# Kernel tuning notes

Measured on AMD Instinct MI355X. Metric: run time of the kernel, lower is better.

## Reference

```python
import jax, jax.numpy as jnp
import numpy as np

N_NODES = 50000
N_EDGES = 800000
IN_CH, HID_CH, OUT_CH = 128, 256, 128


def _linear_init(key, fan_in, fan_out):
    # torch nn.Linear default: U(-1/sqrt(fan_in), 1/sqrt(fan_in)) for W and b
    kw, kb = jax.random.split(key)
    bound = 1.0 / np.sqrt(fan_in)
    W = jax.random.uniform(kw, (fan_in, fan_out), jnp.float32, -bound, bound)
    b = jax.random.uniform(kb, (fan_out,), jnp.float32, -bound, bound)
    return W, b


def setup_inputs() -> dict:
    key = jax.random.key(0)
    ks = jax.random.split(key, 8)
    x = jax.random.normal(ks[0], (N_NODES, IN_CH), jnp.float32)
    edge_index = jax.random.randint(ks[1], (2, N_EDGES), 0, N_NODES, jnp.int64)
    W1a, b1a = _linear_init(ks[2], IN_CH, HID_CH)
    W1b, b1b = _linear_init(ks[3], HID_CH, HID_CH)
    W2, b2 = _linear_init(ks[4], HID_CH, HID_CH)
    W3, b3 = _linear_init(ks[5], HID_CH, OUT_CH)
    eps1 = jnp.zeros((), jnp.float32)  # train_eps=True, init 0
    return {
        "x": x, "edge_index": edge_index,
        "W1a": W1a, "b1a": b1a, "W1b": W1b, "b1b": b1b, "eps1": eps1,
        "W2": W2, "b2": b2, "W3": W3, "b3": b3,
    }


def _gin_aggregate(h, edge_index):
    # PyG: messages flow source (row 0) -> target (row 1); sum aggregation
    src, dst = edge_index[0], edge_index[1]
    return jax.ops.segment_sum(h[src], dst, num_segments=N_NODES)


def reference(x, edge_index, W1a, b1a, W1b, b1b, eps1, W2, b2, W3, b3):
    # conv1: mlp1((1+eps1)*x + sum_neighbors(x)), mlp1 = Lin-ReLU-Lin-ReLU
    z = (1.0 + eps1) * x + _gin_aggregate(x, edge_index)
    h = jax.nn.relu(z @ W1a + b1a)
    h = jax.nn.relu(h @ W1b + b1b)
    h = jax.nn.relu(h)  # outer .relu() (no-op after ReLU, kept for fidelity)
    # conv2: eps fixed at 0 -> (1+0)*h + agg; mlp2 = Lin-ReLU
    z2 = h + _gin_aggregate(h, edge_index)
    h2 = jax.nn.relu(z2 @ W2 + b2)
    h2 = jax.nn.relu(h2)
    return h2 @ W3 + b3
```

## Files before the change

### kernel.cpp

```cpp
#include <hip/hip_runtime.h>


typedef __attribute__((ext_vector_type(8))) short bf16x8;
typedef __attribute__((ext_vector_type(4))) float f32x4;

__device__ __forceinline__ float bf2f(unsigned short u) {
  unsigned v = ((unsigned)u) << 16;
  return __builtin_bit_cast(float, v);
}
__device__ __forceinline__ unsigned short f2bf(float f) {
  unsigned u = __builtin_bit_cast(unsigned, f);
  u += 0x7fffu + ((u >> 16) & 1u);
  return (unsigned short)(u >> 16);
}

__device__ __forceinline__ void async16(const void* g, void* l) {
  __builtin_amdgcn_global_load_lds(
      (const __attribute__((address_space(1))) void*)g,
      (__attribute__((address_space(3))) void*)l, 16, 0, 0);
}

static const int NN     = 50000;
static const int NE     = 800000;
static const int NB_E   = 196;
static const int SCAN_N = 256 * NB_E;
static const int SCAN_NB = 49;
static const int CSR_CAP = 6144;

__global__ __launch_bounds__(256) void k_prep(
    const float* __restrict__ W1a, const float* __restrict__ W1b,
    const float* __restrict__ W2,  const float* __restrict__ W3,
    unsigned short* __restrict__ WT,
    const float* __restrict__ x, unsigned short* __restrict__ xb)
{
  int idx = blockIdx.x * 256 + threadIdx.x;
  if (idx < 196608) {
    const float* W; unsigned short* out; int K, N, li = idx;
    if (li < 32768)        { W = W1a; out = WT;          K = 128; N = 256; }
    else if (li < 98304)   { W = W1b; out = WT + 32768;  K = 256; N = 256; li -= 32768; }
    else if (li < 163840)  { W = W2;  out = WT + 98304;  K = 256; N = 256; li -= 98304; }
    else                   { W = W3;  out = WT + 163840; K = 256; N = 128; li -= 163840; }
    int n = li / K, k = li - n * K;
    out[li] = f2bf(W[k * N + n]);
  } else if (idx < 196608 + NN * 32) {
    int i = idx - 196608;
    float4 v = reinterpret_cast<const float4*>(x)[i];
    ushort4 b; b.x = f2bf(v.x); b.y = f2bf(v.y); b.z = f2bf(v.z); b.w = f2bf(v.w);
    reinterpret_cast<ushort4*>(xb)[i] = b;
  }
}

__global__ __launch_bounds__(256) void k_hist1(const int* __restrict__ ei,
    int* __restrict__ sc)
{
  __shared__ int h[256];
  const int t = threadIdx.x, k = blockIdx.x;
  h[t] = 0;
  __syncthreads();
  const int4* dv4 = reinterpret_cast<const int4*>(ei + NE);
#pragma unroll
  for (int j = 0; j < 4; j++) {
    int e4 = k * 1024 + j * 256 + t;
    if (e4 < NE / 4) {
      int4 d = dv4[e4];
      atomicAdd(&h[d.x >> 8], 1);
      atomicAdd(&h[d.y >> 8], 1);
      atomicAdd(&h[d.z >> 8], 1);
      atomicAdd(&h[d.w >> 8], 1);
    }
  }
  __syncthreads();
  sc[t * NB_E + k] = h[t];
}

__global__ __launch_bounds__(1024) void k_scan_a(int* __restrict__ sc,
    int* __restrict__ bsum)
{
  __shared__ int sh[1024];
  const int t = threadIdx.x;
  int idx = blockIdx.x * 1024 + t;
  int c = (idx < SCAN_N) ? sc[idx] : 0;
  sh[t] = c;
  __syncthreads();
  int v = c;
  for (int off = 1; off < 1024; off <<= 1) {
    int tmp = (t >= off) ? sh[t - off] : 0;
    __syncthreads();
    v += tmp; sh[t] = v;
    __syncthreads();
  }
  if (idx < SCAN_N) sc[idx] = v - c;
  if (t == 1023) bsum[blockIdx.x] = v;
}

__global__ __launch_bounds__(1024) void k_scan_b(const int* __restrict__ bsum,
    int* __restrict__ sc)
{
  __shared__ int sb[64];
  const int t = threadIdx.x;
  if (t < SCAN_NB) sb[t] = bsum[t];
  __syncthreads();
  int base = 0;
  for (int j = 0; j < SCAN_NB; j++) base += (j < (int)blockIdx.x) ? sb[j] : 0;
  int idx = blockIdx.x * 1024 + t;
  if (idx < SCAN_N) sc[idx] += base;
}

__global__ __launch_bounds__(256) void k_binscat(const int* __restrict__ ei,
    const int* __restrict__ sc, int* __restrict__ tmp)
{
  __shared__ int base[256];
  __shared__ int cur[256];
  const int t = threadIdx.x, k = blockIdx.x;
  base[t] = sc[t * NB_E + k];
  cur[t] = 0;
  __syncthreads();
  const int4* sv4 = reinterpret_cast<const int4*>(ei);
  const int4* dv4 = reinterpret_cast<const int4*>(ei + NE);
#pragma unroll
  for (int j = 0; j < 4; j++) {
    int e4 = k * 1024 + j * 256 + t;
    if (e4 < NE / 4) {
      int4 s = sv4[e4];
      int4 d = dv4[e4];
      int b0 = d.x >> 8, p0 = atomicAdd(&cur[b0], 1);
      tmp[base[b0] + p0] = ((d.x & 255) << 16) | s.x;
      int b1 = d.y >> 8, p1 = atomicAdd(&cur[b1], 1);
      tmp[base[b1] + p1] = ((d.y & 255) << 16) | s.y;
      int b2 = d.z >> 8, p2 = atomicAdd(&cur[b2], 1);
      tmp[base[b2] + p2] = ((d.z & 255) << 16) | s.z;
      int b3 = d.w >> 8, p3 = atomicAdd(&cur[b3], 1);
      tmp[base[b3] + p3] = ((d.w & 255) << 16) | s.w;
    }
  }
}

__global__ __launch_bounds__(256) void k_csr(const int* __restrict__ sc,
    const int* __restrict__ tmp, int* __restrict__ offs, int* __restrict__ srcs)
{
  __shared__ int pk[CSR_CAP];
  __shared__ int lh[256];
  __shared__ int lo[256];
  __shared__ int cur[256];
  const int t = threadIdx.x, b = blockIdx.x;
  int ebeg = sc[b * NB_E];
  int eend = sc[(b + 1) * NB_E];
  int cnt = eend - ebeg;
  if (cnt > CSR_CAP) cnt = CSR_CAP;
  lh[t] = 0;
  __syncthreads();
  for (int i = t; i < cnt; i += 256) {
    int v = tmp[ebeg + i];
    pk[i] = v;
    atomicAdd(&lh[(v >> 16) & 255], 1);
  }
  __syncthreads();
  int x = lh[t];
  lo[t] = x;
  __syncthreads();
  for (int off = 1; off < 256; off <<= 1) {
    int y = (t >= off) ? lo[t - off] : 0;
    __syncthreads();
    lo[t] += y;
    __syncthreads();
  }
  int excl = lo[t] - x;
  int g = b * 256 + t;
  if (g <= NN) offs[g] = ebeg + excl;
  cur[t] = excl;
  __syncthreads();
  for (int i = t; i < cnt; i += 256) {
    int v = pk[i];
    int local = (v >> 16) & 255;
    int p = atomicAdd(&cur[local], 1);
    srcs[ebeg + p] = v & 0xFFFF;
  }
}

template<int C, bool L1>
__global__ __launch_bounds__(256) void k_gather(const int* __restrict__ offs,
    const int* __restrict__ srcs, const unsigned short* __restrict__ feat,
    const float* __restrict__ selfx, const float* __restrict__ eps,
    unsigned short* __restrict__ out)
{
  constexpr int TPN = C / 8;
  int tid = blockIdx.x * 256 + threadIdx.x;
  int node = tid / TPN;
  if (node >= NN) return;
  int c0 = (tid % TPN) * 8;

  float a[8];
  if (L1) {
    float sc_ = 1.0f + eps[0];
    const float* sp = selfx + (size_t)node * C + c0;
    f32x4 v0 = __builtin_nontemporal_load(reinterpret_cast<const f32x4*>(sp));
    f32x4 v1 = __builtin_nontemporal_load(reinterpret_cast<const f32x4*>(sp + 4));
    a[0] = v0.x * sc_; a[1] = v0.y * sc_; a[2] = v0.z * sc_; a[3] = v0.w * sc_;
    a[4] = v1.x * sc_; a[5] = v1.y * sc_; a[6] = v1.z * sc_; a[7] = v1.w * sc_;
  } else {
    bf16x8 v = *reinterpret_cast<const bf16x8*>(feat + (size_t)node * C + c0);
#pragma unroll
    for (int j = 0; j < 8; j++) a[j] = bf2f((unsigned short)v[j]);
  }

  int beg = __builtin_nontemporal_load(offs + node);
  int end = __builtin_nontemporal_load(offs + node + 1);
  int i = beg;
  for (; i + 4 <= end; i += 4) {
    int s0 = __builtin_nontemporal_load(srcs + i);
    int s1 = __builtin_nontemporal_load(srcs + i + 1);
    int s2 = __builtin_nontemporal_load(srcs + i + 2);
    int s3 = __builtin_nontemporal_load(srcs + i + 3);
    bf16x8 v0 = *reinterpret_cast<const bf16x8*>(feat + (size_t)s0 * C + c0);
    bf16x8 v1 = *reinterpret_cast<const bf16x8*>(feat + (size_t)s1 * C + c0);
    bf16x8 v2 = *reinterpret_cast<const bf16x8*>(feat + (size_t)s2 * C + c0);
    bf16x8 v3 = *reinterpret_cast<const bf16x8*>(feat + (size_t)s3 * C + c0);
#pragma unroll
    for (int j = 0; j < 8; j++) a[j] += bf2f((unsigned short)v0[j]);
#pragma unroll
    for (int j = 0; j < 8; j++) a[j] += bf2f((unsigned short)v1[j]);
#pragma unroll
    for (int j = 0; j < 8; j++) a[j] += bf2f((unsigned short)v2[j]);
#pragma unroll
    for (int j = 0; j < 8; j++) a[j] += bf2f((unsigned short)v3[j]);
  }
  for (; i < end; ++i) {
    int s0 = __builtin_nontemporal_load(srcs + i);
    bf16x8 v0 = *reinterpret_cast<const bf16x8*>(feat + (size_t)s0 * C + c0);
#pragma unroll
    for (int j = 0; j < 8; j++) a[j] += bf2f((unsigned short)v0[j]);
  }

  bf16x8 o;
#pragma unroll
  for (int j = 0; j < 8; j++) o[j] = (short)f2bf(a[j]);
  __builtin_nontemporal_store(o,
      reinterpret_cast<bf16x8*>(out + (size_t)node * C + c0));
}

template<int CIN, int COUT, bool RELU_OUT, bool OUT_F32>
__global__ __launch_bounds__(1024) void k_mlp(
    const unsigned short* __restrict__ A,
    const unsigned short* __restrict__ B1T,
    const float* __restrict__ bias1,
    const unsigned short* __restrict__ B2T,
    const float* __restrict__ bias2,
    unsigned short* __restrict__ outB, float* __restrict__ outF, int M)
{
  constexpr int LDH = 264;
  __shared__ unsigned short Asb[2][128 * 32];
  __shared__ unsigned short Bsb[2][256 * 32];
  __shared__ unsigned short Hs[128 * LDH];

  const int tid = threadIdx.x;
  const int w = tid >> 6, l = tid & 63;
  const int bm = blockIdx.x * 128;
  const int lr = l >> 2;
  const int lc = (l & 3) * 8;

  auto stageA = [&](int buf, int kt) {
    if (w < 8) {
      int tr = w * 16;
      int ar = bm + tr + lr; if (ar >= M) ar = M - 1;
      async16(A + (size_t)ar * CIN + kt + lc, &Asb[buf][tr * 32]);
    }
    {
      int tr = w * 16;
      async16(B1T + (size_t)(tr + lr) * CIN + kt + lc, &Bsb[buf][tr * 32]);
    }
  };
  auto stageB = [&](int buf, int kt) {
    if (w < COUT / 16) {
      int tr = w * 16;
      async16(B2T + (size_t)(tr + lr) * 256 + kt + lc, &Bsb[buf][tr * 32]);
    }
  };

  const int wrA = w >> 3, wcA = w & 7;
  f32x4 accA[4][2];
#pragma unroll
  for (int m = 0; m < 4; m++)
#pragma unroll
    for (int n = 0; n < 2; n++) accA[m][n] = (f32x4)(0.0f);

  stageA(0, 0);
  __syncthreads();
  int cur = 0;
  for (int kt = 0; kt < CIN; kt += 32) {
    if (kt + 32 < CIN) stageA(cur ^ 1, kt + 32);
    bf16x8 af[4], bfr[2];
#pragma unroll
    for (int m = 0; m < 4; m++)
      af[m] = *reinterpret_cast<const bf16x8*>(
          &Asb[cur][(wrA * 64 + m * 16 + (l & 15)) * 32 + (l >> 4) * 8]);
#pragma unroll
    for (int n = 0; n < 2; n++)
      bfr[n] = *reinterpret_cast<const bf16x8*>(
          &Bsb[cur][(wcA * 32 + n * 16 + (l & 15)) * 32 + (l >> 4) * 8]);
#pragma unroll
    for (int m = 0; m < 4; m++)
#pragma unroll
      for (int n = 0; n < 2; n++)
        accA[m][n] = __builtin_amdgcn_mfma_f32_16x16x32_bf16(
            af[m], bfr[n], accA[m][n], 0, 0, 0);
    __syncthreads();
    cur ^= 1;
  }

  stageB(0, 0);
#pragma unroll
  for (int m = 0; m < 4; m++) {
    int row0 = wrA * 64 + m * 16 + ((l >> 4) << 2);
#pragma unroll
    for (int n = 0; n < 2; n++) {
      int col = wcA * 32 + n * 16 + (l & 15);
      float bv = bias1[col];
#pragma unroll
      for (int r = 0; r < 4; r++) {
        float v = fmaxf(accA[m][n][r] + bv, 0.0f);
        Hs[(row0 + r) * LDH + col] = f2bf(v);
      }
    }
  }
  __syncthreads();

  constexpr int NWC = COUT / 32;
  constexpr int NWR = 16 / NWC;
  constexpr int RPW = 128 / NWR;
  constexpr int MF  = RPW / 16;
  const int wrB = w / NWC, wcB = w % NWC;

  f32x4 accB[MF][2];
#pragma unroll
  for (int m = 0; m < MF; m++)
#pragma unroll
    for (int n = 0; n < 2; n++) accB[m][n] = (f32x4)(0.0f);

  cur = 0;
  for (int kt = 0; kt < 256; kt += 32) {
    if (kt + 32 < 256) stageB(cur ^ 1, kt + 32);
    bf16x8 af[MF], bfr[2];
#pragma unroll
    for (int m = 0; m < MF; m++)
      af[m] = *reinterpret_cast<const bf16x8*>(
          &Hs[(wrB * RPW + m * 16 + (l & 15)) * LDH + kt + (l >> 4) * 8]);
#pragma unroll
    for (int n = 0; n < 2; n++)
      bfr[n] = *reinterpret_cast<const bf16x8*>(
          &Bsb[cur][(wcB * 32 + n * 16 + (l & 15)) * 32 + (l >> 4) * 8]);
#pragma unroll
    for (int m = 0; m < MF; m++)
#pragma unroll
      for (int n = 0; n < 2; n++)
        accB[m][n] = __builtin_amdgcn_mfma_f32_16x16x32_bf16(
            af[m], bfr[n], accB[m][n], 0, 0, 0);
    __syncthreads();
    cur ^= 1;
  }

#pragma unroll
  for (int m = 0; m < MF; m++) {
    int row0 = bm + wrB * RPW + m * 16 + ((l >> 4) << 2);
#pragma unroll
    for (int n = 0; n < 2; n++) {
      int col = wcB * 32 + n * 16 + (l & 15);
      float bv = bias2[col];
#pragma unroll
      for (int r = 0; r < 4; r++) {
        int row = row0 + r;
        if (row < M) {
          float v = accB[m][n][r] + bv;
          if (RELU_OUT) v = fmaxf(v, 0.0f);
          if (OUT_F32) outF[(size_t)row * COUT + col] = v;
          else         outB[(size_t)row * COUT + col] = f2bf(v);
        }
      }
    }
  }
}

static const size_t OFF_XB   = 0;
static const size_t OFF_Z1B  = 12800000;
static const size_t OFF_HB   = 25600000;
static const size_t OFF_Z2B  = 51200000;
static const size_t OFF_SC   = 76800000;
static const size_t OFF_BSUM = 77000704;
static const size_t OFF_TMP  = 77000960;
static const size_t OFF_SRC  = 80200960;
static const size_t OFF_OFFS = 83400960;
static const size_t OFF_WT   = 83601024;

extern "C" void kernel_launch(void* const* d_in, const int* in_sizes, int n_in,
                              void* d_out, int out_size, void* d_ws, size_t ws_size,
                              hipStream_t stream)
{
  const float* x    = (const float*)d_in[0];
  const int*   ei   = (const int*)d_in[1];
  const float* W1a  = (const float*)d_in[2];
  const float* b1a  = (const float*)d_in[3];
  const float* W1b  = (const float*)d_in[4];
  const float* b1b  = (const float*)d_in[5];
  const float* eps1 = (const float*)d_in[6];
  const float* W2   = (const float*)d_in[7];
  const float* b2   = (const float*)d_in[8];
  const float* W3   = (const float*)d_in[9];
  const float* b3   = (const float*)d_in[10];

  char* ws = (char*)d_ws;
  unsigned short* xb   = (unsigned short*)(ws + OFF_XB);
  unsigned short* z1b  = (unsigned short*)(ws + OFF_Z1B);
  unsigned short* hb   = (unsigned short*)(ws + OFF_HB);
  unsigned short* z2b  = (unsigned short*)(ws + OFF_Z2B);
  int*            sc   = (int*)(ws + OFF_SC);
  int*            bsum = (int*)(ws + OFF_BSUM);
  int*            tmp  = (int*)(ws + OFF_TMP);
  int*            srcs = (int*)(ws + OFF_SRC);
  int*            offs = (int*)(ws + OFF_OFFS);
  unsigned short* wt   = (unsigned short*)(ws + OFF_WT);
  unsigned short* w1at = wt;
  unsigned short* w1bt = wt + 32768;
  unsigned short* w2t  = wt + 98304;
  unsigned short* w3t  = wt + 163840;

  k_prep<<<(196608 + NN * 32 + 255) / 256, 256, 0, stream>>>(
      W1a, W1b, W2, W3, wt, x, xb);
  k_hist1<<<NB_E, 256, 0, stream>>>(ei, sc);
  k_scan_a<<<SCAN_NB, 1024, 0, stream>>>(sc, bsum);
  k_scan_b<<<SCAN_NB, 1024, 0, stream>>>(bsum, sc);
  k_binscat<<<NB_E, 256, 0, stream>>>(ei, sc, tmp);
  k_csr<<<NB_E, 256, 0, stream>>>(sc, tmp, offs, srcs);

  k_gather<128, true><<<NN * 16 / 256, 256, 0, stream>>>(
      offs, srcs, xb, x, eps1, z1b);
  k_mlp<128, 256, true, false><<<391, 1024, 0, stream>>>(
      z1b, w1at, b1a, w1bt, b1b, hb, nullptr, NN);

  k_gather<256, false><<<NN * 32 / 256, 256, 0, stream>>>(
      offs, srcs, hb, nullptr, nullptr, z2b);
  k_mlp<256, 128, false, true><<<391, 1024, 0, stream>>>(
      z2b, w2t, b2, w3t, b3, nullptr, (float*)d_out, NN);
}
```

Measured before the change: 193.1 us.

## Fuse histogram into prep, fold scan fixup into consumers, halve MLP tile

Merges the edge-histogram kernel into the weight/feature conversion kernel and removes the separate scan-fixup kernel. Consumers now add the block prefix sums from bsum on the fly, which cuts two launches from the CSR build. The MLP kernels drop to 64-row tiles with 512 threads and twice as many blocks, which lowers shared memory per block and may raise occupancy. In exchange, each block re-reads the B weights for half as many rows, so weight traffic per output row doubles.

```diff
diff --git a/kernel.cpp b/kernel.cpp
--- a/kernel.cpp
+++ b/kernel.cpp
@@ -20,10 +20,10 @@
       (__attribute__((address_space(3))) void*)l, 16, 0, 0);
 }
 
-static const int NN     = 50000;
-static const int NE     = 800000;
-static const int NB_E   = 196;
-static const int SCAN_N = 256 * NB_E;
+static const int NN      = 50000;
+static const int NE      = 800000;
+static const int NB_E    = 196;
+static const int SCAN_N  = 256 * NB_E;
 static const int SCAN_NB = 49;
 static const int CSR_CAP = 6144;
 
@@ -31,9 +31,32 @@
     const float* __restrict__ W1a, const float* __restrict__ W1b,
     const float* __restrict__ W2,  const float* __restrict__ W3,
     unsigned short* __restrict__ WT,
-    const float* __restrict__ x, unsigned short* __restrict__ xb)
-{
-  int idx = blockIdx.x * 256 + threadIdx.x;
+    const float* __restrict__ x, unsigned short* __restrict__ xb,
+    const int* __restrict__ ei, int* __restrict__ sc)
+{
+  __shared__ int h[256];
+  const int t = threadIdx.x;
+  if (blockIdx.x < NB_E) {
+    const int k = blockIdx.x;
+    h[t] = 0;
+    __syncthreads();
+    const int4* dv4 = reinterpret_cast<const int4*>(ei + NE);
+#pragma unroll
+    for (int j = 0; j < 4; j++) {
+      int e4 = k * 1024 + j * 256 + t;
+      if (e4 < NE / 4) {
+        int4 d = dv4[e4];
+        atomicAdd(&h[d.x >> 8], 1);
+        atomicAdd(&h[d.y >> 8], 1);
+        atomicAdd(&h[d.z >> 8], 1);
+        atomicAdd(&h[d.w >> 8], 1);
+      }
+    }
+    __syncthreads();
+    sc[t * NB_E + k] = h[t];
+    return;
+  }
+  int idx = (blockIdx.x - NB_E) * 256 + t;
   if (idx < 196608) {
     const float* W; unsigned short* out; int K, N, li = idx;
     if (li < 32768)        { W = W1a; out = WT;          K = 128; N = 256; }
@@ -50,29 +73,6 @@
   }
 }
 
-__global__ __launch_bounds__(256) void k_hist1(const int* __restrict__ ei,
-    int* __restrict__ sc)
-{
-  __shared__ int h[256];
-  const int t = threadIdx.x, k = blockIdx.x;
-  h[t] = 0;
-  __syncthreads();
-  const int4* dv4 = reinterpret_cast<const int4*>(ei + NE);
-#pragma unroll
-  for (int j = 0; j < 4; j++) {
-    int e4 = k * 1024 + j * 256 + t;
-    if (e4 < NE / 4) {
-      int4 d = dv4[e4];
-      atomicAdd(&h[d.x >> 8], 1);
-      atomicAdd(&h[d.y >> 8], 1);
-      atomicAdd(&h[d.z >> 8], 1);
-      atomicAdd(&h[d.w >> 8], 1);
-    }
-  }
-  __syncthreads();
-  sc[t * NB_E + k] = h[t];
-}
-
 __global__ __launch_bounds__(1024) void k_scan_a(int* __restrict__ sc,
     int* __restrict__ bsum)
 {
@@ -93,27 +93,24 @@
   if (t == 1023) bsum[blockIdx.x] = v;
 }
 
-__global__ __launch_bounds__(1024) void k_scan_b(const int* __restrict__ bsum,
-    int* __restrict__ sc)
-{
-  __shared__ int sb[64];
-  const int t = threadIdx.x;
-  if (t < SCAN_NB) sb[t] = bsum[t];
-  __syncthreads();
-  int base = 0;
-  for (int j = 0; j < SCAN_NB; j++) base += (j < (int)blockIdx.x) ? sb[j] : 0;
-  int idx = blockIdx.x * 1024 + t;
-  if (idx < SCAN_N) sc[idx] += base;
-}
-
 __global__ __launch_bounds__(256) void k_binscat(const int* __restrict__ ei,
-    const int* __restrict__ sc, int* __restrict__ tmp)
+    const int* __restrict__ sc, const int* __restrict__ bsum,
+    int* __restrict__ tmp)
 {
   __shared__ int base[256];
   __shared__ int cur[256];
+  __shared__ int sb[SCAN_NB];
   const int t = threadIdx.x, k = blockIdx.x;
-  base[t] = sc[t * NB_E + k];
+  if (t < SCAN_NB) sb[t] = bsum[t];
   cur[t] = 0;
+  __syncthreads();
+  {
+    int idx = t * NB_E + k;
+    int nb = idx >> 10;
+    int pre = 0;
+    for (int j = 0; j < nb; j++) pre += sb[j];
+    base[t] = sc[idx] + pre;
+  }
   __syncthreads();
   const int4* sv4 = reinterpret_cast<const int4*>(ei);
   const int4* dv4 = reinterpret_cast<const int4*>(ei + NE);
@@ -136,18 +133,28 @@
 }
 
 __global__ __launch_bounds__(256) void k_csr(const int* __restrict__ sc,
-    const int* __restrict__ tmp, int* __restrict__ offs, int* __restrict__ srcs)
+    const int* __restrict__ bsum, const int* __restrict__ tmp,
+    int* __restrict__ offs, int* __restrict__ srcs)
 {
   __shared__ int pk[CSR_CAP];
   __shared__ int lh[256];
   __shared__ int lo[256];
   __shared__ int cur[256];
+  __shared__ int sb[SCAN_NB];
   const int t = threadIdx.x, b = blockIdx.x;
-  int ebeg = sc[b * NB_E];
-  int eend = sc[(b + 1) * NB_E];
+  if (t < SCAN_NB) sb[t] = bsum[t];
+  lh[t] = 0;
+  __syncthreads();
+  int i0 = b * NB_E, i1 = (b + 1) * NB_E;
+  int p0 = 0, p1 = 0;
+  for (int j = 0; j < SCAN_NB; j++) {
+    p0 += (j < (i0 >> 10)) ? sb[j] : 0;
+    p1 += (j < (i1 >> 10)) ? sb[j] : 0;
+  }
+  int ebeg = sc[i0] + p0;
+  int eend = sc[i1] + p1;
   int cnt = eend - ebeg;
   if (cnt > CSR_CAP) cnt = CSR_CAP;
-  lh[t] = 0;
   __syncthreads();
   for (int i = t; i < cnt; i += 256) {
     int v = tmp[ebeg + i];
@@ -171,8 +178,7 @@
   __syncthreads();
   for (int i = t; i < cnt; i += 256) {
     int v = pk[i];
-    int local = (v >> 16) & 255;
-    int p = atomicAdd(&cur[local], 1);
+    int p = atomicAdd(&cur[(v >> 16) & 255], 1);
     srcs[ebeg + p] = v & 0xFFFF;
   }
 }
@@ -239,7 +245,7 @@
 }
 
 template<int CIN, int COUT, bool RELU_OUT, bool OUT_F32>
-__global__ __launch_bounds__(1024) void k_mlp(
+__global__ __launch_bounds__(512) void k_mlp(
     const unsigned short* __restrict__ A,
     const unsigned short* __restrict__ B1T,
     const float* __restrict__ bias1,
@@ -248,35 +254,36 @@
     unsigned short* __restrict__ outB, float* __restrict__ outF, int M)
 {
   constexpr int LDH = 264;
-  __shared__ unsigned short Asb[2][128 * 32];
+  __shared__ unsigned short Asb[2][64 * 32];
   __shared__ unsigned short Bsb[2][256 * 32];
-  __shared__ unsigned short Hs[128 * LDH];
+  __shared__ unsigned short Hs[64 * LDH];
 
   const int tid = threadIdx.x;
   const int w = tid >> 6, l = tid & 63;
-  const int bm = blockIdx.x * 128;
+  const int bm = blockIdx.x * 64;
   const int lr = l >> 2;
   const int lc = (l & 3) * 8;
 
   auto stageA = [&](int buf, int kt) {
-    if (w < 8) {
+    if (w < 4) {
       int tr = w * 16;
       int ar = bm + tr + lr; if (ar >= M) ar = M - 1;
       async16(A + (size_t)ar * CIN + kt + lc, &Asb[buf][tr * 32]);
     }
-    {
-      int tr = w * 16;
+#pragma unroll
+    for (int ch = w; ch < 16; ch += 8) {
+      int tr = ch * 16;
       async16(B1T + (size_t)(tr + lr) * CIN + kt + lc, &Bsb[buf][tr * 32]);
     }
   };
   auto stageB = [&](int buf, int kt) {
-    if (w < COUT / 16) {
-      int tr = w * 16;
+#pragma unroll
+    for (int ch = w; ch < COUT / 16; ch += 8) {
+      int tr = ch * 16;
       async16(B2T + (size_t)(tr + lr) * 256 + kt + lc, &Bsb[buf][tr * 32]);
     }
   };
 
-  const int wrA = w >> 3, wcA = w & 7;
   f32x4 accA[4][2];
 #pragma unroll
   for (int m = 0; m < 4; m++)
@@ -292,11 +299,11 @@
 #pragma unroll
     for (int m = 0; m < 4; m++)
       af[m] = *reinterpret_cast<const bf16x8*>(
-          &Asb[cur][(wrA * 64 + m * 16 + (l & 15)) * 32 + (l >> 4) * 8]);
+          &Asb[cur][(m * 16 + (l & 15)) * 32 + (l >> 4) * 8]);
 #pragma unroll
     for (int n = 0; n < 2; n++)
       bfr[n] = *reinterpret_cast<const bf16x8*>(
-          &Bsb[cur][(wcA * 32 + n * 16 + (l & 15)) * 32 + (l >> 4) * 8]);
+          &Bsb[cur][(w * 32 + n * 16 + (l & 15)) * 32 + (l >> 4) * 8]);
 #pragma unroll
     for (int m = 0; m < 4; m++)
 #pragma unroll
@@ -310,10 +317,10 @@
   stageB(0, 0);
 #pragma unroll
   for (int m = 0; m < 4; m++) {
-    int row0 = wrA * 64 + m * 16 + ((l >> 4) << 2);
+    int row0 = m * 16 + ((l >> 4) << 2);
 #pragma unroll
     for (int n = 0; n < 2; n++) {
-      int col = wcA * 32 + n * 16 + (l & 15);
+      int col = w * 32 + n * 16 + (l & 15);
       float bv = bias1[col];
 #pragma unroll
       for (int r = 0; r < 4; r++) {
@@ -325,8 +332,8 @@
   __syncthreads();
 
   constexpr int NWC = COUT / 32;
-  constexpr int NWR = 16 / NWC;
-  constexpr int RPW = 128 / NWR;
+  constexpr int NWR = 8 / NWC;
+  constexpr int RPW = 64 / NWR;
   constexpr int MF  = RPW / 16;
   const int wrB = w / NWC, wcB = w % NWC;
 
@@ -422,21 +429,19 @@
   unsigned short* w2t  = wt + 98304;
   unsigned short* w3t  = wt + 163840;
 
-  k_prep<<<(196608 + NN * 32 + 255) / 256, 256, 0, stream>>>(
-      W1a, W1b, W2, W3, wt, x, xb);
-  k_hist1<<<NB_E, 256, 0, stream>>>(ei, sc);
+  k_prep<<<NB_E + (196608 + NN * 32 + 255) / 256, 256, 0, stream>>>(
+      W1a, W1b, W2, W3, wt, x, xb, ei, sc);
   k_scan_a<<<SCAN_NB, 1024, 0, stream>>>(sc, bsum);
-  k_scan_b<<<SCAN_NB, 1024, 0, stream>>>(bsum, sc);
-  k_binscat<<<NB_E, 256, 0, stream>>>(ei, sc, tmp);
-  k_csr<<<NB_E, 256, 0, stream>>>(sc, tmp, offs, srcs);
+  k_binscat<<<NB_E, 256, 0, stream>>>(ei, sc, bsum, tmp);
+  k_csr<<<NB_E, 256, 0, stream>>>(sc, bsum, tmp, offs, srcs);
 
   k_gather<128, true><<<NN * 16 / 256, 256, 0, stream>>>(
       offs, srcs, xb, x, eps1, z1b);
-  k_mlp<128, 256, true, false><<<391, 1024, 0, stream>>>(
+  k_mlp<128, 256, true, false><<<782, 512, 0, stream>>>(
       z1b, w1at, b1a, w1bt, b1b, hb, nullptr, NN);
 
   k_gather<256, false><<<NN * 32 / 256, 256, 0, stream>>>(
       offs, srcs, hb, nullptr, nullptr, z2b);
-  k_mlp<256, 128, false, true><<<391, 1024, 0, stream>>>(
+  k_mlp<256, 128, false, true><<<782, 512, 0, stream>>>(
       z2b, w2t, b2, w3t, b3, nullptr, (float*)d_out, NN);
 }
```

New measurement: 191.5 us. About the same (-0.8%).
